# Performance work log

Measured on AMD Instinct MI355X. Metric: run time of the kernel, lower is better.

## Reference

```python
import jax, jax.numpy as jnp
import numpy as np

N, H, E, ED = 8192, 128, 16384, 16
MLP_HID = 64


def setup_inputs() -> dict:
    key = jax.random.key(0)
    ks = jax.random.split(key, 10)
    h = jax.random.normal(ks[0], (N, H), dtype=jnp.float32)
    edge_index = jax.random.randint(ks[1], (2, E), 0, N, dtype=jnp.int32)
    edge_features = jax.random.normal(ks[2], (E, ED), dtype=jnp.float32)
    # edge MLP params (Linear stored as [in, out] for x @ W + b)
    W1 = jax.random.normal(ks[3], (ED, MLP_HID), dtype=jnp.float32) / np.sqrt(ED)
    b1 = jnp.zeros((MLP_HID,), dtype=jnp.float32)
    W2 = jax.random.normal(ks[4], (MLP_HID, H * H), dtype=jnp.float32) / np.sqrt(MLP_HID)
    b2 = jnp.zeros((H * H,), dtype=jnp.float32)
    # GRUCell params (torch layout: [3H, in]) with gate order r, z, n
    W_ih = jax.random.normal(ks[5], (3 * H, H), dtype=jnp.float32) / np.sqrt(H)
    W_hh = jax.random.normal(ks[6], (3 * H, H), dtype=jnp.float32) / np.sqrt(H)
    b_ih = jax.random.normal(ks[7], (3 * H,), dtype=jnp.float32) * 0.01
    b_hh = jax.random.normal(ks[8], (3 * H,), dtype=jnp.float32) * 0.01
    return {"h": h, "edge_index": edge_index, "edge_features": edge_features,
            "W1": W1, "b1": b1, "W2": W2, "b2": b2,
            "W_ih": W_ih, "W_hh": W_hh, "b_ih": b_ih, "b_hh": b_hh}


def _gru_cell(x, h, W_ih, W_hh, b_ih, b_hh):
    hd = h.shape[1]
    gi = x @ W_ih.T + b_ih          # [N, 3H]
    gh = h @ W_hh.T + b_hh          # [N, 3H]
    r = jax.nn.sigmoid(gi[:, :hd] + gh[:, :hd])
    z = jax.nn.sigmoid(gi[:, hd:2 * hd] + gh[:, hd:2 * hd])
    n = jnp.tanh(gi[:, 2 * hd:] + r * gh[:, 2 * hd:])
    return (1.0 - z) * n + z * h


def reference(h, edge_index, edge_features, W1, b1, W2, b2, W_ih, W_hh, b_ih, b_hh):
    hd = h.shape[1]
    src = edge_index[0]
    tgt = edge_index[1]
    h_w = h[src]                                          # [E, H] gather
    A = jax.nn.relu(edge_features @ W1 + b1) @ W2 + b2    # [E, H*H]
    A = A.reshape(-1, hd, hd)                             # [E, H, H]
    messages = jnp.einsum('eij,ej->ei', A, h_w)           # batched matvec
    m = jax.ops.segment_sum(messages, tgt, num_segments=h.shape[0])  # scatter_add
    return _gru_cell(m, h, W_ih, W_hh, b_ih, b_hh)
```

## Files before the change

kernel.cpp:

```cpp
#include <hip/hip_runtime.h>

#define N_NODES 8192
#define H_DIM   128
#define E_EDGES 16384
#define ED_DIM  16
#define MLP_HID 64

typedef __attribute__((ext_vector_type(8))) _Float16 half8;
typedef __attribute__((ext_vector_type(2))) _Float16 half2v;
typedef __attribute__((ext_vector_type(4))) float f32x4;

__device__ __forceinline__ unsigned short f2h(float f) {
  _Float16 v = (_Float16)f;
  return __builtin_bit_cast(unsigned short, v);
}

__device__ __forceinline__ void glds16(const void* g, void* l) {
  __builtin_amdgcn_global_load_lds(
      (const __attribute__((address_space(1))) unsigned int*)g,
      (__attribute__((address_space(3))) unsigned int*)l, 16, 0, 0);
}

__device__ __forceinline__ unsigned mul_pk(unsigned u, half2v r2) {
  half2v a = __builtin_bit_cast(half2v, u);
  half2v p = a * r2;
  return __builtin_bit_cast(unsigned, p);
}

__device__ __forceinline__ float sigmoidf_fast(float x) {
  return 1.f / (1.f + __expf(-x));
}
__device__ __forceinline__ float tanhf_fast(float x) {
  float t = __expf(-2.f * fabsf(x));
  float r = (1.f - t) / (1.f + t);
  return copysignf(r, x);
}

__global__ __launch_bounds__(256) void prep_kernel(
    const float* __restrict__ h, const float* __restrict__ ef,
    const float* __restrict__ W1, const float* __restrict__ b1,
    const float* __restrict__ W2, const float* __restrict__ W_ih,
    const float* __restrict__ W_hh, unsigned short* __restrict__ hb,
    unsigned short* __restrict__ relu1h, unsigned short* __restrict__ w2sw,
    unsigned short* __restrict__ wih_sw, unsigned short* __restrict__ whh_sw,
    float* __restrict__ m_ws) {
  const int bid = blockIdx.x, tid = threadIdx.x;
  if (bid < 1024) {
    int i4 = (bid * 256 + tid) * 4;
    float4 v = *(const float4*)(h + i4);
    unsigned short o[4] = {f2h(v.x), f2h(v.y), f2h(v.z), f2h(v.w)};
    *(uint2*)(hb + i4) = *(const uint2*)o;
  } else if (bid < 1088) {
    __shared__ float W1s[ED_DIM * MLP_HID];
    __shared__ float b1s[MLP_HID];
    {
      float4 w = *(const float4*)(W1 + tid * 4);
      *(float4*)(W1s + tid * 4) = w;
      if (tid < MLP_HID) b1s[tid] = b1[tid];
    }
    int e = (bid - 1024) * 256 + tid;
    float efr[ED_DIM];
#pragma unroll
    for (int j4 = 0; j4 < 4; ++j4) {
      float4 v = *(const float4*)(ef + e * ED_DIM + j4 * 4);
      efr[j4 * 4 + 0] = v.x;
      efr[j4 * 4 + 1] = v.y;
      efr[j4 * 4 + 2] = v.z;
      efr[j4 * 4 + 3] = v.w;
    }
    __syncthreads();
    unsigned short o[MLP_HID];
#pragma unroll 4
    for (int k = 0; k < MLP_HID; ++k) {
      float v = b1s[k];
#pragma unroll
      for (int j = 0; j < ED_DIM; ++j) v += efr[j] * W1s[j * MLP_HID + k];
      o[k] = f2h(fmaxf(v, 0.0f));
    }
#pragma unroll
    for (int q = 0; q < 8; ++q)
      *(uint4*)(relu1h + e * 64 + q * 8) = *(const uint4*)(o + q * 8);
  } else if (bid < 1600) {
    int c = (bid - 1088) * 256 + tid;
    int k = c >> 11;
    int rem = c & 2047;
    int col = rem >> 4;
    int jq = rem & 15;
    int g = col >> 5, cc = col & 31;
    const float* s = W2 + (size_t)c * 8;
    unsigned short q[8];
#pragma unroll
    for (int jj = 0; jj < 8; ++jj) q[jj] = f2h(s[jj]);
    int dest = ((k * 4 + g) * 16 + jq) * 32 + cc;
    *(uint4*)(w2sw + (size_t)dest * 8) = *(const uint4*)q;
  } else if (bid < 1648) {
    int c = (bid - 1600) * 256 + tid;
    int mat = c >= 6144;
    int cc = mat ? c - 6144 : c;
    int kl = cc / 1536;
    int rem = cc - kl * 1536;
    int q = rem / 384;
    int j = rem - q * 384;
    int g = (j % 48) >> 4;
    int u = (j / 48) * 16 + (j & 15);
    const float* W = mat ? W_hh : W_ih;
    const float* s = W + (g * 128 + u) * H_DIM + kl * 32 + q * 8;
    unsigned short o[8];
#pragma unroll
    for (int kk = 0; kk < 8; ++kk) o[kk] = f2h(s[kk]);
    unsigned short* dst = mat ? whh_sw : wih_sw;
    *(uint4*)(dst + cc * 8) = *(const uint4*)o;
  } else {
    int idx = (bid - 1648) * 256 + tid;
    float4 z = {0.f, 0.f, 0.f, 0.f};
    float4* p = (float4*)(m_ws + (size_t)idx * 16);
    p[0] = z; p[1] = z; p[2] = z; p[3] = z;
  }
}

__global__ __launch_bounds__(256, 2) void edge_gemm_scatter(
    const unsigned short* __restrict__ hb, const unsigned short* __restrict__ relu1h,
    const unsigned short* __restrict__ w2sw, const int* __restrict__ src,
    const int* __restrict__ tgt, float* __restrict__ m_ws) {
  const int tid = threadIdx.x;
  const int bx = blockIdx.x;
  const int s_half = bx & 1;
  const int g = (bx >> 1) & 3;
  const int e0 = (bx >> 3) * 256;
  const int n0 = g * 32;
  const int kl0 = s_half * 32;

  __shared__ __align__(16) unsigned short sh_r[256 * 40];
  __shared__ __align__(16) unsigned short sh_b[4][4096];

  const int lane = tid & 63, wave = tid >> 6;
  const int l15 = lane & 15, quad = lane >> 4;

#pragma unroll
  for (int i = 0; i < 4; ++i) {
    int c = i * 256 + tid;
    int e = c >> 2, part = c & 3;
    uint4 v = *(const uint4*)(relu1h + (e0 + e) * 64 + s_half * 32 + part * 8);
    *(uint4*)(sh_r + e * 40 + part * 8) = v;
  }
#pragma unroll
  for (int p = 0; p < 3; ++p) {
#pragma unroll
    for (int i = 0; i < 2; ++i) {
      int s = i * 256 + tid;
      glds16(w2sw + ((size_t)((kl0 + p) * 4 + g)) * 4096 + s * 8,
             sh_b[p] + s * 8);
    }
  }

  uint4 a_h[4][4];
#pragma unroll
  for (int mi = 0; mi < 4; ++mi) {
    int s = src[e0 + wave * 64 + mi * 16 + l15];
    const unsigned short* row = hb + s * H_DIM;
#pragma unroll
    for (int t = 0; t < 4; ++t)
      a_h[mi][t] = *(const uint4*)(row + t * 32 + quad * 8);
  }

  f32x4 acc[4][2];
#pragma unroll
  for (int a = 0; a < 4; ++a)
#pragma unroll
    for (int b = 0; b < 2; ++b) {
      f32x4 z = {0.f, 0.f, 0.f, 0.f};
      acc[a][b] = z;
    }

  __syncthreads();

  half8 rr[4];
  for (int i = 0; i < 32; ++i) {
    asm volatile("s_waitcnt vmcnt(4)" ::: "memory");
    __builtin_amdgcn_s_barrier();
    asm volatile("" ::: "memory");
    {
      int pf = (i + 3) & 31;
      const unsigned short* gsrc =
          w2sw + ((size_t)((kl0 + pf) * 4 + g)) * 4096;
      unsigned short* d = sh_b[(i + 3) & 3];
#pragma unroll
      for (int j = 0; j < 2; ++j) {
        int s = j * 256 + tid;
        glds16(gsrc + s * 8, d + s * 8);
      }
    }
    const unsigned short* curb = sh_b[i & 3];
    if ((i & 7) == 0) {
      int oct = i >> 3;
#pragma unroll
      for (int mi = 0; mi < 4; ++mi)
        rr[mi] = *(const half8*)(sh_r + (wave * 64 + mi * 16 + l15) * 40 + oct * 8);
    }
    const int kb = i & 7;
    half2v rvh[4];
#pragma unroll
    for (int mi = 0; mi < 4; ++mi) {
      _Float16 rh = rr[mi][kb];
      half2v r2 = {rh, rh};
      rvh[mi] = r2;
    }
#pragma unroll
    for (int t = 0; t < 4; ++t) {
      half8 b0 = *(const half8*)(curb + ((t * 4 + quad) * 32 + l15) * 8);
      half8 b1 = *(const half8*)(curb + ((t * 4 + quad) * 32 + 16 + l15) * 8);
#pragma unroll
      for (int mi = 0; mi < 4; ++mi) {
        uint4 hq = a_h[mi][t];
        uint4 o;
        o.x = mul_pk(hq.x, rvh[mi]);
        o.y = mul_pk(hq.y, rvh[mi]);
        o.z = mul_pk(hq.z, rvh[mi]);
        o.w = mul_pk(hq.w, rvh[mi]);
        half8 af = __builtin_bit_cast(half8, o);
        acc[mi][0] = __builtin_amdgcn_mfma_f32_16x16x32_f16(af, b0, acc[mi][0], 0, 0, 0);
        acc[mi][1] = __builtin_amdgcn_mfma_f32_16x16x32_f16(af, b1, acc[mi][1], 0, 0, 0);
      }
    }
  }

  asm volatile("s_waitcnt vmcnt(0)" ::: "memory");

#pragma unroll
  for (int mi = 0; mi < 4; ++mi) {
#pragma unroll
    for (int r = 0; r < 4; ++r) {
      int e = e0 + wave * 64 + mi * 16 + quad * 4 + r;
      int trow = tgt[e];
      float* dst = m_ws + trow * H_DIM + n0 + l15;
      atomicAdd(dst, acc[mi][0][r]);
      atomicAdd(dst + 16, acc[mi][1][r]);
    }
  }
}

__global__ __launch_bounds__(256) void gru_mfma(
    const float* __restrict__ m_ws, const unsigned short* __restrict__ hb,
    const float* __restrict__ h, const unsigned short* __restrict__ wih_sw,
    const unsigned short* __restrict__ whh_sw, const float* __restrict__ b_ih,
    const float* __restrict__ b_hh, float* __restrict__ out) {
  const int tid = threadIdx.x;
  const int mt = blockIdx.x >> 2, nt = blockIdx.x & 3;
  const int node0 = mt * 128, j0 = nt * 96;

  __shared__ __align__(16) unsigned short Am[128 * 136];
  __shared__ __align__(16) unsigned short Ah[128 * 136];
  __shared__ __align__(16) unsigned short Bi[12288];
  __shared__ __align__(16) unsigned short Bh[12288];

#pragma unroll
  for (int i = 0; i < 6; ++i) {
    int s = i * 256 + tid;
    int kq = s / 96, jc = s - kq * 96;
    glds16(wih_sw + (kq * 384 + j0 + jc) * 8, Bi + s * 8);
    glds16(whh_sw + (kq * 384 + j0 + jc) * 8, Bh + s * 8);
  }
#pragma unroll
  for (int i = 0; i < 8; ++i) {
    int c = i * 256 + tid;
    int row = c >> 4, c8 = c & 15;
    float4 v0 = *(const float4*)(m_ws + (node0 + row) * H_DIM + c8 * 8);
    float4 v1 = *(const float4*)(m_ws + (node0 + row) * H_DIM + c8 * 8 + 4);
    unsigned short o[8] = {f2h(v0.x), f2h(v0.y), f2h(v0.z), f2h(v0.w),
                           f2h(v1.x), f2h(v1.y), f2h(v1.z), f2h(v1.w)};
    *(uint4*)(Am + row * 136 + c8 * 8) = *(const uint4*)o;
    *(uint4*)(Ah + row * 136 + c8 * 8) =
        *(const uint4*)(hb + (node0 + row) * H_DIM + c8 * 8);
  }
  __syncthreads();

  const int lane = tid & 63, wave = tid >> 6;
  const int wm = wave >> 1, wn = wave & 1;
  const int l15 = lane & 15, quad = lane >> 4;

  f32x4 gi[4][3], gh[4][3];
#pragma unroll
  for (int a = 0; a < 4; ++a)
#pragma unroll
    for (int b = 0; b < 3; ++b) {
      f32x4 z = {0.f, 0.f, 0.f, 0.f};
      gi[a][b] = z;
      gh[a][b] = z;
    }

#pragma unroll
  for (int kl = 0; kl < 4; ++kl) {
    half8 am[4], ah[4];
#pragma unroll
    for (int mi = 0; mi < 4; ++mi) {
      int row = wm * 64 + mi * 16 + l15;
      am[mi] = *(const half8*)(Am + row * 136 + kl * 32 + quad * 8);
      ah[mi] = *(const half8*)(Ah + row * 136 + kl * 32 + quad * 8);
    }
    half8 bi[3], bh[3];
#pragma unroll
    for (int g = 0; g < 3; ++g) {
      int off = ((kl * 4 + quad) * 96 + wn * 48 + g * 16 + l15) * 8;
      bi[g] = *(const half8*)(Bi + off);
      bh[g] = *(const half8*)(Bh + off);
    }
#pragma unroll
    for (int mi = 0; mi < 4; ++mi)
#pragma unroll
      for (int g = 0; g < 3; ++g) {
        gi[mi][g] = __builtin_amdgcn_mfma_f32_16x16x32_f16(am[mi], bi[g],
                                                           gi[mi][g], 0, 0, 0);
        gh[mi][g] = __builtin_amdgcn_mfma_f32_16x16x32_f16(ah[mi], bh[g],
                                                           gh[mi][g], 0, 0, 0);
      }
  }

  const int u = nt * 32 + wn * 16 + l15;
  const float bir = b_ih[u], bhr = b_hh[u];
  const float biz = b_ih[128 + u], bhz = b_hh[128 + u];
  const float bin = b_ih[256 + u], bhn = b_hh[256 + u];
#pragma unroll
  for (int mi = 0; mi < 4; ++mi) {
#pragma unroll
    for (int r = 0; r < 4; ++r) {
      int row = node0 + wm * 64 + mi * 16 + quad * 4 + r;
      float xr = gi[mi][0][r] + gh[mi][0][r] + bir + bhr;
      float xz = gi[mi][1][r] + gh[mi][1][r] + biz + bhz;
      float xn = gi[mi][2][r] + bin;
      float hn = gh[mi][2][r] + bhn;
      float rg = sigmoidf_fast(xr);
      float zg = sigmoidf_fast(xz);
      float ng = tanhf_fast(xn + rg * hn);
      float hv = h[row * H_DIM + u];
      out[row * H_DIM + u] = (1.f - zg) * ng + zg * hv;
    }
  }
}

extern "C" void kernel_launch(void* const* d_in, const int* in_sizes, int n_in,
                              void* d_out, int out_size, void* d_ws, size_t ws_size,
                              hipStream_t stream) {
  (void)in_sizes; (void)n_in; (void)out_size; (void)ws_size;
  const float* h    = (const float*)d_in[0];
  const int*   ei   = (const int*)d_in[1];
  const float* ef   = (const float*)d_in[2];
  const float* W1   = (const float*)d_in[3];
  const float* b1   = (const float*)d_in[4];
  const float* W2   = (const float*)d_in[5];
  const float* W_ih = (const float*)d_in[7];
  const float* W_hh = (const float*)d_in[8];
  const float* b_ih = (const float*)d_in[9];
  const float* b_hh = (const float*)d_in[10];

  char* ws = (char*)d_ws;
  float*          m_ws   = (float*)(ws + 0);
  unsigned short* hb     = (unsigned short*)(ws + 4194304);
  unsigned short* relu1h = (unsigned short*)(ws + 6291456);
  unsigned short* w2sw   = (unsigned short*)(ws + 8388608);
  unsigned short* wih_sw = (unsigned short*)(ws + 10485760);
  unsigned short* whh_sw = (unsigned short*)(ws + 10584064);

  prep_kernel<<<1904, 256, 0, stream>>>(h, ef, W1, b1, W2, W_ih, W_hh,
                                        hb, relu1h, w2sw, wih_sw, whh_sw, m_ws);
  edge_gemm_scatter<<<512, 256, 0, stream>>>(hb, relu1h, w2sw, ei,
                                             ei + E_EDGES, m_ws);
  gru_mfma<<<256, 256, 0, stream>>>(m_ws, hb, h, wih_sw, whh_sw, b_ih, b_hh,
                                    (float*)d_out);
}
```

Measured before the change: 139.0 us.

## Replace atomic scatter-add with CSR gather of fp16 per-edge messages

Drops the float atomicAdd scatter into a zeroed node buffer. Edges are now bucketed by target with a degree count, a single-block prefix scan and a fill pass. The edge GEMM writes packed fp16 messages per edge for each K-half, and the GRU kernel gathers and sums each node's incoming messages in fp32 before its MFMA. This removes atomic contention and the memset of the accumulator, at the cost of three extra small launches, a serial one-block scan, irregular gathers in the GRU load phase, and fp16 rounding of the partial messages.

```diff
diff --git a/kernel.cpp b/kernel.cpp
--- a/kernel.cpp
+++ b/kernel.cpp
@@ -40,10 +40,11 @@
     const float* __restrict__ h, const float* __restrict__ ef,
     const float* __restrict__ W1, const float* __restrict__ b1,
     const float* __restrict__ W2, const float* __restrict__ W_ih,
-    const float* __restrict__ W_hh, unsigned short* __restrict__ hb,
+    const float* __restrict__ W_hh, const int* __restrict__ tgt,
+    unsigned short* __restrict__ hb,
     unsigned short* __restrict__ relu1h, unsigned short* __restrict__ w2sw,
     unsigned short* __restrict__ wih_sw, unsigned short* __restrict__ whh_sw,
-    float* __restrict__ m_ws) {
+    int* __restrict__ deg) {
   const int bid = blockIdx.x, tid = threadIdx.x;
   if (bid < 1024) {
     int i4 = (bid * 256 + tid) * 4;
@@ -91,7 +92,8 @@
     unsigned short q[8];
 #pragma unroll
     for (int jj = 0; jj < 8; ++jj) q[jj] = f2h(s[jj]);
-    int dest = ((k * 4 + g) * 16 + jq) * 32 + cc;
+    int newc = (cc >> 1) + (cc & 1) * 16;
+    int dest = ((k * 4 + g) * 16 + jq) * 32 + newc;
     *(uint4*)(w2sw + (size_t)dest * 8) = *(const uint4*)q;
   } else if (bid < 1648) {
     int c = (bid - 1600) * 256 + tid;
@@ -111,17 +113,56 @@
     unsigned short* dst = mat ? whh_sw : wih_sw;
     *(uint4*)(dst + cc * 8) = *(const uint4*)o;
   } else {
-    int idx = (bid - 1648) * 256 + tid;
-    float4 z = {0.f, 0.f, 0.f, 0.f};
-    float4* p = (float4*)(m_ws + (size_t)idx * 16);
-    p[0] = z; p[1] = z; p[2] = z; p[3] = z;
-  }
+    int e = (bid - 1648) * 256 + tid;
+    atomicAdd(&deg[tgt[e]], 1);
+  }
+}
+
+__global__ __launch_bounds__(256) void scan_kernel(const int* __restrict__ deg,
+                                                   int* __restrict__ offset,
+                                                   int* __restrict__ cursor) {
+  __shared__ int ts[256];
+  const int tid = threadIdx.x;
+  const int base = tid * 32;
+  int local[32];
+  int s = 0;
+#pragma unroll
+  for (int j = 0; j < 32; ++j) {
+    local[j] = deg[base + j];
+    s += local[j];
+  }
+  ts[tid] = s;
+  __syncthreads();
+  for (int off = 1; off < 256; off <<= 1) {
+    int v = ts[tid];
+    int add = (tid >= off) ? ts[tid - off] : 0;
+    __syncthreads();
+    ts[tid] = v + add;
+    __syncthreads();
+  }
+  int run = (tid == 0) ? 0 : ts[tid - 1];
+#pragma unroll
+  for (int j = 0; j < 32; ++j) {
+    offset[base + j] = run;
+    cursor[base + j] = run;
+    run += local[j];
+  }
+  if (tid == 255) offset[8192] = run;
+}
+
+__global__ __launch_bounds__(256) void fill_kernel(const int* __restrict__ tgt,
+                                                   int* __restrict__ cursor,
+                                                   int* __restrict__ elist) {
+  int e = blockIdx.x * 256 + threadIdx.x;
+  int t = tgt[e];
+  int pos = atomicAdd(&cursor[t], 1);
+  elist[pos] = e;
 }
 
 __global__ __launch_bounds__(256, 2) void edge_gemm_scatter(
     const unsigned short* __restrict__ hb, const unsigned short* __restrict__ relu1h,
     const unsigned short* __restrict__ w2sw, const int* __restrict__ src,
-    const int* __restrict__ tgt, float* __restrict__ m_ws) {
+    unsigned short* __restrict__ msg0, unsigned short* __restrict__ msg1) {
   const int tid = threadIdx.x;
   const int bx = blockIdx.x;
   const int s_half = bx & 1;
@@ -226,21 +267,24 @@
 
   asm volatile("s_waitcnt vmcnt(0)" ::: "memory");
 
+  unsigned short* msg = s_half ? msg1 : msg0;
 #pragma unroll
   for (int mi = 0; mi < 4; ++mi) {
 #pragma unroll
     for (int r = 0; r < 4; ++r) {
       int e = e0 + wave * 64 + mi * 16 + quad * 4 + r;
-      int trow = tgt[e];
-      float* dst = m_ws + trow * H_DIM + n0 + l15;
-      atomicAdd(dst, acc[mi][0][r]);
-      atomicAdd(dst + 16, acc[mi][1][r]);
+      unsigned short h0 = f2h(acc[mi][0][r]);
+      unsigned short h1 = f2h(acc[mi][1][r]);
+      unsigned v = (unsigned)h0 | ((unsigned)h1 << 16);
+      *(unsigned*)(msg + (size_t)e * H_DIM + n0 + 2 * l15) = v;
     }
   }
 }
 
 __global__ __launch_bounds__(256) void gru_mfma(
-    const float* __restrict__ m_ws, const unsigned short* __restrict__ hb,
+    const int* __restrict__ offset, const int* __restrict__ elist,
+    const unsigned short* __restrict__ msg0, const unsigned short* __restrict__ msg1,
+    const unsigned short* __restrict__ hb,
     const float* __restrict__ h, const unsigned short* __restrict__ wih_sw,
     const unsigned short* __restrict__ whh_sw, const float* __restrict__ b_ih,
     const float* __restrict__ b_hh, float* __restrict__ out) {
@@ -264,13 +308,22 @@
   for (int i = 0; i < 8; ++i) {
     int c = i * 256 + tid;
     int row = c >> 4, c8 = c & 15;
-    float4 v0 = *(const float4*)(m_ws + (node0 + row) * H_DIM + c8 * 8);
-    float4 v1 = *(const float4*)(m_ws + (node0 + row) * H_DIM + c8 * 8 + 4);
-    unsigned short o[8] = {f2h(v0.x), f2h(v0.y), f2h(v0.z), f2h(v0.w),
-                           f2h(v1.x), f2h(v1.y), f2h(v1.z), f2h(v1.w)};
+    int r = node0 + row;
+    int beg = offset[r], end = offset[r + 1];
+    float s[8] = {0.f, 0.f, 0.f, 0.f, 0.f, 0.f, 0.f, 0.f};
+    for (int idx = beg; idx < end; ++idx) {
+      int e = elist[idx];
+      half8 v0 = *(const half8*)(msg0 + (size_t)e * H_DIM + c8 * 8);
+      half8 v1 = *(const half8*)(msg1 + (size_t)e * H_DIM + c8 * 8);
+#pragma unroll
+      for (int j = 0; j < 8; ++j) s[j] += (float)v0[j] + (float)v1[j];
+    }
+    unsigned short o[8];
+#pragma unroll
+    for (int j = 0; j < 8; ++j) o[j] = f2h(s[j]);
     *(uint4*)(Am + row * 136 + c8 * 8) = *(const uint4*)o;
     *(uint4*)(Ah + row * 136 + c8 * 8) =
-        *(const uint4*)(hb + (node0 + row) * H_DIM + c8 * 8);
+        *(const uint4*)(hb + (size_t)(node0 + row) * H_DIM + c8 * 8);
   }
   __syncthreads();
 
@@ -353,17 +406,26 @@
   const float* b_hh = (const float*)d_in[10];
 
   char* ws = (char*)d_ws;
-  float*          m_ws   = (float*)(ws + 0);
-  unsigned short* hb     = (unsigned short*)(ws + 4194304);
-  unsigned short* relu1h = (unsigned short*)(ws + 6291456);
-  unsigned short* w2sw   = (unsigned short*)(ws + 8388608);
-  unsigned short* wih_sw = (unsigned short*)(ws + 10485760);
-  unsigned short* whh_sw = (unsigned short*)(ws + 10584064);
-
-  prep_kernel<<<1904, 256, 0, stream>>>(h, ef, W1, b1, W2, W_ih, W_hh,
-                                        hb, relu1h, w2sw, wih_sw, whh_sw, m_ws);
-  edge_gemm_scatter<<<512, 256, 0, stream>>>(hb, relu1h, w2sw, ei,
-                                             ei + E_EDGES, m_ws);
-  gru_mfma<<<256, 256, 0, stream>>>(m_ws, hb, h, wih_sw, whh_sw, b_ih, b_hh,
-                                    (float*)d_out);
-}
+  unsigned short* msg0   = (unsigned short*)(ws + 0);
+  unsigned short* msg1   = (unsigned short*)(ws + 4194304);
+  unsigned short* hb     = (unsigned short*)(ws + 8388608);
+  unsigned short* relu1h = (unsigned short*)(ws + 10485760);
+  unsigned short* w2sw   = (unsigned short*)(ws + 12582912);
+  unsigned short* wih_sw = (unsigned short*)(ws + 14680064);
+  unsigned short* whh_sw = (unsigned short*)(ws + 14778368);
+  int*            deg    = (int*)(ws + 14876672);
+  int*            offset = (int*)(ws + 14909440);
+  int*            cursor = (int*)(ws + 14946304);
+  int*            elist  = (int*)(ws + 14979072);
+
+  const int* tgt = ei + E_EDGES;
+
+  hipMemsetAsync(deg, 0, 8192 * sizeof(int), stream);
+  prep_kernel<<<1712, 256, 0, stream>>>(h, ef, W1, b1, W2, W_ih, W_hh, tgt,
+                                        hb, relu1h, w2sw, wih_sw, whh_sw, deg);
+  scan_kernel<<<1, 256, 0, stream>>>(deg, offset, cursor);
+  fill_kernel<<<64, 256, 0, stream>>>(tgt, cursor, elist);
+  edge_gemm_scatter<<<512, 256, 0, stream>>>(hb, relu1h, w2sw, ei, msg0, msg1);
+  gru_mfma<<<256, 256, 0, stream>>>(offset, elist, msg0, msg1, hb, h,
+                                    wih_sw, whh_sw, b_ih, b_hh, (float*)d_out);
+}
```

After: 161.1 us. +15.9%, slower.

## Accumulate messages with packed fp16 atomics and widen GRU blocks to 512 threads

Applied to the files above, without the earlier changes.

The scatter now converts each pair of accumulator values to fp16 and issues one global_atomic_pk_add_f16 per pair instead of two fp32 atomicAdds. W2 columns are permuted so each lane holds adjacent output columns. The message buffer becomes fp16, which halves its zeroing and read traffic and lets the GRU kernel load it directly without conversion. The GRU kernel moves to 512 threads with half the rows per wave. Accumulating in fp16 atomics risks precision loss and overflow when many edges hit the same node.

```diff
diff --git a/kernel.cpp b/kernel.cpp
--- a/kernel.cpp
+++ b/kernel.cpp
@@ -9,6 +9,7 @@
 typedef __attribute__((ext_vector_type(8))) _Float16 half8;
 typedef __attribute__((ext_vector_type(2))) _Float16 half2v;
 typedef __attribute__((ext_vector_type(4))) float f32x4;
+typedef __attribute__((ext_vector_type(4))) unsigned int u32x4;
 
 __device__ __forceinline__ unsigned short f2h(float f) {
   _Float16 v = (_Float16)f;
@@ -43,7 +44,7 @@
     const float* __restrict__ W_hh, unsigned short* __restrict__ hb,
     unsigned short* __restrict__ relu1h, unsigned short* __restrict__ w2sw,
     unsigned short* __restrict__ wih_sw, unsigned short* __restrict__ whh_sw,
-    float* __restrict__ m_ws) {
+    unsigned short* __restrict__ m_ws) {
   const int bid = blockIdx.x, tid = threadIdx.x;
   if (bid < 1024) {
     int i4 = (bid * 256 + tid) * 4;
@@ -91,7 +92,8 @@
     unsigned short q[8];
 #pragma unroll
     for (int jj = 0; jj < 8; ++jj) q[jj] = f2h(s[jj]);
-    int dest = ((k * 4 + g) * 16 + jq) * 32 + cc;
+    int newc = (cc >> 1) + (cc & 1) * 16;
+    int dest = ((k * 4 + g) * 16 + jq) * 32 + newc;
     *(uint4*)(w2sw + (size_t)dest * 8) = *(const uint4*)q;
   } else if (bid < 1648) {
     int c = (bid - 1600) * 256 + tid;
@@ -112,8 +114,8 @@
     *(uint4*)(dst + cc * 8) = *(const uint4*)o;
   } else {
     int idx = (bid - 1648) * 256 + tid;
-    float4 z = {0.f, 0.f, 0.f, 0.f};
-    float4* p = (float4*)(m_ws + (size_t)idx * 16);
+    uint4 z = {0u, 0u, 0u, 0u};
+    uint4* p = (uint4*)(m_ws + (size_t)idx * 32);
     p[0] = z; p[1] = z; p[2] = z; p[3] = z;
   }
 }
@@ -121,7 +123,7 @@
 __global__ __launch_bounds__(256, 2) void edge_gemm_scatter(
     const unsigned short* __restrict__ hb, const unsigned short* __restrict__ relu1h,
     const unsigned short* __restrict__ w2sw, const int* __restrict__ src,
-    const int* __restrict__ tgt, float* __restrict__ m_ws) {
+    const int* __restrict__ tgt, unsigned short* __restrict__ m_ws) {
   const int tid = threadIdx.x;
   const int bx = blockIdx.x;
   const int s_half = bx & 1;
@@ -232,15 +234,18 @@
     for (int r = 0; r < 4; ++r) {
       int e = e0 + wave * 64 + mi * 16 + quad * 4 + r;
       int trow = tgt[e];
-      float* dst = m_ws + trow * H_DIM + n0 + l15;
-      atomicAdd(dst, acc[mi][0][r]);
-      atomicAdd(dst + 16, acc[mi][1][r]);
-    }
-  }
-}
-
-__global__ __launch_bounds__(256) void gru_mfma(
-    const float* __restrict__ m_ws, const unsigned short* __restrict__ hb,
+      unsigned short h0 = f2h(acc[mi][0][r]);
+      unsigned short h1 = f2h(acc[mi][1][r]);
+      unsigned pv = (unsigned)h0 | ((unsigned)h1 << 16);
+      unsigned short* dst = m_ws + (size_t)trow * H_DIM + n0 + 2 * l15;
+      asm volatile("global_atomic_pk_add_f16 %0, %1, off"
+                   :: "v"(dst), "v"(pv) : "memory");
+    }
+  }
+}
+
+__global__ __launch_bounds__(512) void gru_mfma(
+    const unsigned short* __restrict__ m_ws, const unsigned short* __restrict__ hb,
     const float* __restrict__ h, const unsigned short* __restrict__ wih_sw,
     const unsigned short* __restrict__ whh_sw, const float* __restrict__ b_ih,
     const float* __restrict__ b_hh, float* __restrict__ out) {
@@ -254,23 +259,20 @@
   __shared__ __align__(16) unsigned short Bh[12288];
 
 #pragma unroll
-  for (int i = 0; i < 6; ++i) {
-    int s = i * 256 + tid;
+  for (int i = 0; i < 3; ++i) {
+    int s = i * 512 + tid;
     int kq = s / 96, jc = s - kq * 96;
     glds16(wih_sw + (kq * 384 + j0 + jc) * 8, Bi + s * 8);
     glds16(whh_sw + (kq * 384 + j0 + jc) * 8, Bh + s * 8);
   }
 #pragma unroll
-  for (int i = 0; i < 8; ++i) {
-    int c = i * 256 + tid;
+  for (int i = 0; i < 4; ++i) {
+    int c = i * 512 + tid;
     int row = c >> 4, c8 = c & 15;
-    float4 v0 = *(const float4*)(m_ws + (node0 + row) * H_DIM + c8 * 8);
-    float4 v1 = *(const float4*)(m_ws + (node0 + row) * H_DIM + c8 * 8 + 4);
-    unsigned short o[8] = {f2h(v0.x), f2h(v0.y), f2h(v0.z), f2h(v0.w),
-                           f2h(v1.x), f2h(v1.y), f2h(v1.z), f2h(v1.w)};
-    *(uint4*)(Am + row * 136 + c8 * 8) = *(const uint4*)o;
+    *(uint4*)(Am + row * 136 + c8 * 8) =
+        *(const uint4*)(m_ws + (size_t)(node0 + row) * H_DIM + c8 * 8);
     *(uint4*)(Ah + row * 136 + c8 * 8) =
-        *(const uint4*)(hb + (node0 + row) * H_DIM + c8 * 8);
+        *(const uint4*)(hb + (size_t)(node0 + row) * H_DIM + c8 * 8);
   }
   __syncthreads();
 
@@ -278,9 +280,9 @@
   const int wm = wave >> 1, wn = wave & 1;
   const int l15 = lane & 15, quad = lane >> 4;
 
-  f32x4 gi[4][3], gh[4][3];
-#pragma unroll
-  for (int a = 0; a < 4; ++a)
+  f32x4 gi[2][3], gh[2][3];
+#pragma unroll
+  for (int a = 0; a < 2; ++a)
 #pragma unroll
     for (int b = 0; b < 3; ++b) {
       f32x4 z = {0.f, 0.f, 0.f, 0.f};
@@ -290,10 +292,10 @@
 
 #pragma unroll
   for (int kl = 0; kl < 4; ++kl) {
-    half8 am[4], ah[4];
-#pragma unroll
-    for (int mi = 0; mi < 4; ++mi) {
-      int row = wm * 64 + mi * 16 + l15;
+    half8 am[2], ah[2];
+#pragma unroll
+    for (int mi = 0; mi < 2; ++mi) {
+      int row = wm * 32 + mi * 16 + l15;
       am[mi] = *(const half8*)(Am + row * 136 + kl * 32 + quad * 8);
       ah[mi] = *(const half8*)(Ah + row * 136 + kl * 32 + quad * 8);
     }
@@ -305,7 +307,7 @@
       bh[g] = *(const half8*)(Bh + off);
     }
 #pragma unroll
-    for (int mi = 0; mi < 4; ++mi)
+    for (int mi = 0; mi < 2; ++mi)
 #pragma unroll
       for (int g = 0; g < 3; ++g) {
         gi[mi][g] = __builtin_amdgcn_mfma_f32_16x16x32_f16(am[mi], bi[g],
@@ -320,10 +322,10 @@
   const float biz = b_ih[128 + u], bhz = b_hh[128 + u];
   const float bin = b_ih[256 + u], bhn = b_hh[256 + u];
 #pragma unroll
-  for (int mi = 0; mi < 4; ++mi) {
+  for (int mi = 0; mi < 2; ++mi) {
 #pragma unroll
     for (int r = 0; r < 4; ++r) {
-      int row = node0 + wm * 64 + mi * 16 + quad * 4 + r;
+      int row = node0 + wm * 32 + mi * 16 + quad * 4 + r;
       float xr = gi[mi][0][r] + gh[mi][0][r] + bir + bhr;
       float xz = gi[mi][1][r] + gh[mi][1][r] + biz + bhz;
       float xn = gi[mi][2][r] + bin;
@@ -353,17 +355,17 @@
   const float* b_hh = (const float*)d_in[10];
 
   char* ws = (char*)d_ws;
-  float*          m_ws   = (float*)(ws + 0);
-  unsigned short* hb     = (unsigned short*)(ws + 4194304);
-  unsigned short* relu1h = (unsigned short*)(ws + 6291456);
-  unsigned short* w2sw   = (unsigned short*)(ws + 8388608);
-  unsigned short* wih_sw = (unsigned short*)(ws + 10485760);
-  unsigned short* whh_sw = (unsigned short*)(ws + 10584064);
-
-  prep_kernel<<<1904, 256, 0, stream>>>(h, ef, W1, b1, W2, W_ih, W_hh,
+  unsigned short* m_ws   = (unsigned short*)(ws + 0);
+  unsigned short* hb     = (unsigned short*)(ws + 2097152);
+  unsigned short* relu1h = (unsigned short*)(ws + 4194304);
+  unsigned short* w2sw   = (unsigned short*)(ws + 6291456);
+  unsigned short* wih_sw = (unsigned short*)(ws + 8388608);
+  unsigned short* whh_sw = (unsigned short*)(ws + 8486912);
+
+  prep_kernel<<<1776, 256, 0, stream>>>(h, ef, W1, b1, W2, W_ih, W_hh,
                                         hb, relu1h, w2sw, wih_sw, whh_sw, m_ws);
   edge_gemm_scatter<<<512, 256, 0, stream>>>(hb, relu1h, w2sw, ei,
                                              ei + E_EDGES, m_ws);
-  gru_mfma<<<256, 256, 0, stream>>>(m_ws, hb, h, wih_sw, whh_sw, b_ih, b_hh,
+  gru_mfma<<<256, 512, 0, stream>>>(m_ws, hb, h, wih_sw, whh_sw, b_ih, b_hh,
                                     (float*)d_out);
 }
```

Measured after the change: 133.9 us. -3.7%, faster.
